# Performance work log

Measured on AMD Instinct MI355X. Metric: run time of the kernel, lower is better.

The kernel has to match this reference:

```python
import jax, jax.numpy as jnp
import numpy as np

TEMPERATURE = 0.1
EPS = 1e-12  # matches torch F.normalize default eps


def setup_inputs() -> dict:
    key = jax.random.key(0)
    k1, k2 = jax.random.split(key)
    B, D = 4096, 512
    features1 = jax.random.normal(k1, (B, D), dtype=jnp.float32)
    features2 = jax.random.normal(k2, (B, D), dtype=jnp.float32)
    return {"features1": features1, "features2": features2}


def _l2_normalize(x, axis=1):
    norm = jnp.linalg.norm(x, axis=axis, keepdims=True)
    return x / jnp.maximum(norm, EPS)


def reference(features1, features2):
    B = features1.shape[0]
    f1 = _l2_normalize(features1)
    f2 = _l2_normalize(features2)
    features = jnp.concatenate([f1, f2], axis=0)  # (2B, D)
    sim = jnp.matmul(features, features.T) / TEMPERATURE  # (2B, 2B)
    # mask self-similarity on the diagonal with -inf
    diag = jnp.eye(2 * B, dtype=bool)
    sim = jnp.where(diag, -jnp.inf, sim)
    # positive pair labels: row i pairs with i+B (first half) / i-B (second half)
    labels = jnp.concatenate([jnp.arange(B) + B, jnp.arange(B)], axis=0)
    log_probs = jax.nn.log_softmax(sim, axis=-1)  # (2B, 2B)
    nll = -jnp.take_along_axis(log_probs, labels[:, None], axis=1)[:, 0]
    return jnp.mean(nll)
```

## Files before the change

### kernel.cpp

```cpp
#include <hip/hip_runtime.h>

#define NROWS 8192
#define HALF_N 4096
#define DIM 512
#define INV_T 10.0f
#define NRB 64
#define NBLOCKS 2080

typedef __attribute__((ext_vector_type(4))) float f32x4;
typedef __attribute__((ext_vector_type(2))) long long2v;

__device__ __forceinline__ void async16(const void* g, void* l) {
  __builtin_amdgcn_global_load_lds(
      (const __attribute__((address_space(1))) unsigned int*)g,
      (__attribute__((address_space(3))) unsigned int*)l, 16, 0, 0);
}

__global__ __launch_bounds__(256) void norm_cast_k(
    const float* __restrict__ f1, const float* __restrict__ f2,
    unsigned char* __restrict__ Fa, unsigned char* __restrict__ Fb,
    float* __restrict__ rowsum, float* __restrict__ out) {
  int wave = threadIdx.x >> 6;
  int lane = threadIdx.x & 63;
  int row = blockIdx.x * 4 + wave;
  const float* src = (row < HALF_N) ? (f1 + (size_t)row * DIM)
                                    : (f2 + (size_t)(row - HALF_N) * DIM);
  const float4* p = reinterpret_cast<const float4*>(src + lane * 8);
  float4 v0 = p[0];
  float4 v1 = p[1];
  float ss = v0.x*v0.x + v0.y*v0.y + v0.z*v0.z + v0.w*v0.w
           + v1.x*v1.x + v1.y*v1.y + v1.z*v1.z + v1.w*v1.w;
  #pragma unroll
  for (int off = 1; off < 64; off <<= 1) ss += __shfl_xor(ss, off);
  float scale = 1.0f / fmaxf(sqrtf(ss), 1e-12f);
  int lo = __builtin_amdgcn_cvt_pk_fp8_f32(v0.x * scale, v0.y * scale, 0, false);
  lo = __builtin_amdgcn_cvt_pk_fp8_f32(v0.z * scale, v0.w * scale, lo, true);
  int hi = __builtin_amdgcn_cvt_pk_fp8_f32(v1.x * scale, v1.y * scale, 0, false);
  hi = __builtin_amdgcn_cvt_pk_fp8_f32(v1.z * scale, v1.w * scale, hi, true);
  int2 val = make_int2(lo, hi);
  int u = lane & 7;
  int g = lane >> 3;
  int pos = 2 * (u & 3) + (u >> 2);
  *reinterpret_cast<int2*>(Fb + (size_t)row * DIM + g * 64 + pos * 8) = val;
  int chunk = g * 4 + (u & 3);
  int slot = u >> 2;
  *reinterpret_cast<int2*>(Fa + (size_t)(row >> 4) * 8192 + chunk * 256 +
                           (row & 15) * 16 + slot * 8) = val;
  if (lane == 0) rowsum[row] = 0.0f;
  if (blockIdx.x == 0 && threadIdx.x == 0) out[0] = 0.0f;
}

__global__ __launch_bounds__(256, 3) void sym_gemm_k(
    const unsigned char* __restrict__ Fa, const unsigned char* __restrict__ Fb,
    float* __restrict__ rowsum, float* __restrict__ pairsim) {
  int bx = blockIdx.x;
  int gbx = (bx & 7) * (NBLOCKS / 8) + (bx >> 3);
  int rb = 0, rem = gbx;
  while (rem >= NRB - rb) { rem -= NRB - rb; ++rb; }
  const int cb = rb + rem;
  const int row0 = rb * 128, col0 = cb * 128;

  const int tid = threadIdx.x;
  const int wave = tid >> 6;
  const int lane = tid & 63;
  const int quad = lane >> 4;
  const int colid = lane & 15;
  const int wr0 = (wave >> 1) * 64;
  const int wc0 = (wave & 1) * 64;

  __shared__ __align__(16) unsigned char Blds[2][128 * 64];
  __shared__ float redrow[128];
  __shared__ float redcol[128];

  if (tid < 128) { redrow[tid] = 0.0f; redcol[tid] = 0.0f; }

  const unsigned char* srcB[2]; int dstO[2];
  #pragma unroll
  for (int seg = 0; seg < 2; ++seg) {
    int inst = wave + seg * 4;
    int r = inst * 16 + (lane >> 2);
    int c = (lane & 3) ^ ((r >> 1) & 3);
    srcB[seg] = Fb + (size_t)(col0 + r) * DIM + c * 16;
    dstO[seg] = inst * 1024;
  }

  const unsigned char* agp[4];
  #pragma unroll
  for (int t = 0; t < 4; ++t)
    agp[t] = Fa + (size_t)((row0 + wr0 + t * 16) >> 4) * 8192 +
             quad * 256 + colid * 16;

  int boff[4];
  #pragma unroll
  for (int t = 0; t < 4; ++t) {
    int rc = wc0 + t * 16 + colid;
    boff[t] = rc * 64 + ((quad ^ ((rc >> 1) & 3)) << 4);
  }

  f32x4 acc[4][4];
  #pragma unroll
  for (int t = 0; t < 4; ++t)
    #pragma unroll
    for (int u = 0; u < 4; ++u) acc[t][u] = (f32x4){0.f, 0.f, 0.f, 0.f};

  #pragma unroll
  for (int seg = 0; seg < 2; ++seg)
    async16(srcB[seg], &Blds[0][0] + dstO[seg]);
  long2v afc[4];
  #pragma unroll
  for (int t = 0; t < 4; ++t)
    afc[t] = *reinterpret_cast<const long2v*>(agp[t]);
  __syncthreads();

  #pragma unroll
  for (int kc = 0; kc < 8; ++kc) {
    const int cur = kc & 1;
    if (kc < 7) {
      #pragma unroll
      for (int seg = 0; seg < 2; ++seg)
        async16(srcB[seg] + (kc + 1) * 64, &Blds[cur ^ 1][0] + dstO[seg]);
    }
    long2v afn[4];
    if (kc < 7) {
      #pragma unroll
      for (int t = 0; t < 4; ++t)
        afn[t] = *reinterpret_cast<const long2v*>(agp[t] + (kc + 1) * 1024);
    }

    long2v bf[4];
    #pragma unroll
    for (int u = 0; u < 4; ++u)
      bf[u] = *reinterpret_cast<const long2v*>(&Blds[cur][0] + boff[u]);
    #pragma unroll
    for (int s = 0; s < 2; ++s)
      #pragma unroll
      for (int t = 0; t < 4; ++t)
        #pragma unroll
        for (int u = 0; u < 4; ++u)
          acc[t][u] = __builtin_amdgcn_mfma_f32_16x16x32_fp8_fp8(
              afc[t][s], bf[u][s], acc[t][u], 0, 0, 0);

    __syncthreads();
    if (kc < 7) {
      #pragma unroll
      for (int t = 0; t < 4; ++t) afc[t] = afn[t];
    }
  }

  float re[4][4];
  float ce[4];
  #pragma unroll
  for (int t = 0; t < 4; ++t)
    #pragma unroll
    for (int r = 0; r < 4; ++r) re[t][r] = 0.0f;
  #pragma unroll
  for (int u = 0; u < 4; ++u) ce[u] = 0.0f;

  #pragma unroll
  for (int t = 0; t < 4; ++t) {
    #pragma unroll
    for (int u = 0; u < 4; ++u) {
      f32x4 a = acc[t][u];
      const int gc = col0 + wc0 + u * 16 + colid;
      #pragma unroll
      for (int r = 0; r < 4; ++r) {
        int grow = row0 + wr0 + t * 16 + quad * 4 + r;
        float sim = a[r] * INV_T;
        float e = (gc > grow) ? __expf(sim) : 0.0f;
        re[t][r] += e;
        ce[u] += e;
        if (gc == grow + HALF_N && grow < HALF_N) {
          pairsim[grow] = sim;
          pairsim[gc] = sim;
        }
      }
    }
  }

  #pragma unroll
  for (int t = 0; t < 4; ++t)
    #pragma unroll
    for (int r = 0; r < 4; ++r) {
      float v = re[t][r];
      v += __shfl_xor(v, 1); v += __shfl_xor(v, 2);
      v += __shfl_xor(v, 4); v += __shfl_xor(v, 8);
      if (colid == 0) atomicAdd(&redrow[wr0 + t * 16 + quad * 4 + r], v);
    }
  #pragma unroll
  for (int u = 0; u < 4; ++u) {
    float v = ce[u];
    v += __shfl_xor(v, 16); v += __shfl_xor(v, 32);
    if (lane < 16) atomicAdd(&redcol[wc0 + u * 16 + colid], v);
  }
  __syncthreads();
  if (tid < 128) atomicAdd(&rowsum[row0 + tid], redrow[tid]);
  else           atomicAdd(&rowsum[col0 + tid - 128], redcol[tid - 128]);
}

__global__ __launch_bounds__(256) void finalize_k(
    const float* __restrict__ rowsum, const float* __restrict__ pairsim,
    float* __restrict__ out) {
  int i = blockIdx.x * 256 + threadIdx.x;
  float local = logf(rowsum[i]) - pairsim[i];
  #pragma unroll
  for (int off = 1; off < 64; off <<= 1) local += __shfl_xor(local, off);
  if ((threadIdx.x & 63) == 0)
    atomicAdd(out, local * (1.0f / (float)NROWS));
}

extern "C" void kernel_launch(void* const* d_in, const int* in_sizes, int n_in,
                              void* d_out, int out_size, void* d_ws, size_t ws_size,
                              hipStream_t stream) {
  const float* f1 = (const float*)d_in[0];
  const float* f2 = (const float*)d_in[1];
  unsigned char* Fa = (unsigned char*)d_ws;
  unsigned char* Fb = Fa + (size_t)NROWS * DIM;
  float* rowsum = (float*)(Fb + (size_t)NROWS * DIM);
  float* pairsim = rowsum + NROWS;
  float* out = (float*)d_out;

  norm_cast_k<<<NROWS / 4, 256, 0, stream>>>(f1, f2, Fa, Fb, rowsum, out);
  sym_gemm_k<<<NBLOCKS, 256, 0, stream>>>(Fa, Fb, rowsum, pairsim);
  finalize_k<<<NROWS / 256, 256, 0, stream>>>(rowsum, pairsim, out);
}
```

Baseline: 108.6 us.

## Enlarge symmetric GEMM tiles to 256x128 with 8 waves and 128-wide K chunks

Result: slower. 115.9 us (+6.7%).

```diff
diff --git a/kernel.cpp b/kernel.cpp
--- a/kernel.cpp
+++ b/kernel.cpp
@@ -4,8 +4,7 @@
 #define HALF_N 4096
 #define DIM 512
 #define INV_T 10.0f
-#define NRB 64
-#define NBLOCKS 2080
+#define NBLOCKS 1056
 
 typedef __attribute__((ext_vector_type(4))) float f32x4;
 typedef __attribute__((ext_vector_type(2))) long long2v;
@@ -50,15 +49,15 @@
   if (blockIdx.x == 0 && threadIdx.x == 0) out[0] = 0.0f;
 }
 
-__global__ __launch_bounds__(256, 3) void sym_gemm_k(
+__global__ __launch_bounds__(512, 4) void sym_gemm_k(
     const unsigned char* __restrict__ Fa, const unsigned char* __restrict__ Fb,
     float* __restrict__ rowsum, float* __restrict__ pairsim) {
   int bx = blockIdx.x;
   int gbx = (bx & 7) * (NBLOCKS / 8) + (bx >> 3);
   int rb = 0, rem = gbx;
-  while (rem >= NRB - rb) { rem -= NRB - rb; ++rb; }
-  const int cb = rb + rem;
-  const int row0 = rb * 128, col0 = cb * 128;
+  while (rem >= 64 - 2 * rb) { rem -= 64 - 2 * rb; ++rb; }
+  const int cb = 2 * rb + rem;
+  const int row0 = rb * 256, col0 = cb * 128;
 
   const int tid = threadIdx.x;
   const int wave = tid >> 6;
@@ -68,20 +67,23 @@
   const int wr0 = (wave >> 1) * 64;
   const int wc0 = (wave & 1) * 64;
 
-  __shared__ __align__(16) unsigned char Blds[2][128 * 64];
-  __shared__ float redrow[128];
+  __shared__ __align__(16) unsigned char Blds[2][128 * 128];
+  __shared__ float redrow[256];
   __shared__ float redcol[128];
 
-  if (tid < 128) { redrow[tid] = 0.0f; redcol[tid] = 0.0f; }
+  if (tid < 256) redrow[tid] = 0.0f;
+  if (tid < 128) redcol[tid] = 0.0f;
 
   const unsigned char* srcB[2]; int dstO[2];
-  #pragma unroll
-  for (int seg = 0; seg < 2; ++seg) {
-    int inst = wave + seg * 4;
-    int r = inst * 16 + (lane >> 2);
-    int c = (lane & 3) ^ ((r >> 1) & 3);
-    srcB[seg] = Fb + (size_t)(col0 + r) * DIM + c * 16;
-    dstO[seg] = inst * 1024;
+  {
+    int rloc = lane >> 3;
+    int l = (lane & 7) ^ rloc;
+    #pragma unroll
+    for (int seg = 0; seg < 2; ++seg) {
+      int inst = wave + seg * 8;
+      srcB[seg] = Fb + (size_t)(col0 + inst * 8 + rloc) * DIM + l * 16;
+      dstO[seg] = inst * 1024;
+    }
   }
 
   const unsigned char* agp[4];
@@ -90,11 +92,11 @@
     agp[t] = Fa + (size_t)((row0 + wr0 + t * 16) >> 4) * 8192 +
              quad * 256 + colid * 16;
 
-  int boff[4];
-  #pragma unroll
-  for (int t = 0; t < 4; ++t) {
-    int rc = wc0 + t * 16 + colid;
-    boff[t] = rc * 64 + ((quad ^ ((rc >> 1) & 3)) << 4);
+  int bq[4];
+  #pragma unroll
+  for (int u = 0; u < 4; ++u) {
+    int rc = wc0 + u * 16 + colid;
+    bq[u] = rc * 128 + ((quad ^ (colid & 7)) << 4);
   }
 
   f32x4 acc[4][4];
@@ -106,44 +108,35 @@
   #pragma unroll
   for (int seg = 0; seg < 2; ++seg)
     async16(srcB[seg], &Blds[0][0] + dstO[seg]);
-  long2v afc[4];
-  #pragma unroll
-  for (int t = 0; t < 4; ++t)
-    afc[t] = *reinterpret_cast<const long2v*>(agp[t]);
-  __syncthreads();
-
-  #pragma unroll
-  for (int kc = 0; kc < 8; ++kc) {
-    const int cur = kc & 1;
-    if (kc < 7) {
+
+  #pragma unroll
+  for (int kc = 0; kc < 4; ++kc) {
+    __syncthreads();
+    if (kc < 3) {
       #pragma unroll
       for (int seg = 0; seg < 2; ++seg)
-        async16(srcB[seg] + (kc + 1) * 64, &Blds[cur ^ 1][0] + dstO[seg]);
-    }
-    long2v afn[4];
-    if (kc < 7) {
+        async16(srcB[seg] + (kc + 1) * 128, &Blds[(kc & 1) ^ 1][0] + dstO[seg]);
+    }
+    #pragma unroll
+    for (int h = 0; h < 2; ++h) {
+      const int ss = kc * 2 + h;
+      long2v af[4];
       #pragma unroll
       for (int t = 0; t < 4; ++t)
-        afn[t] = *reinterpret_cast<const long2v*>(agp[t] + (kc + 1) * 1024);
-    }
-
-    long2v bf[4];
-    #pragma unroll
-    for (int u = 0; u < 4; ++u)
-      bf[u] = *reinterpret_cast<const long2v*>(&Blds[cur][0] + boff[u]);
-    #pragma unroll
-    for (int s = 0; s < 2; ++s)
-      #pragma unroll
-      for (int t = 0; t < 4; ++t)
+        af[t] = *reinterpret_cast<const long2v*>(agp[t] + ss * 1024);
+      long2v bf[4];
+      #pragma unroll
+      for (int u = 0; u < 4; ++u)
+        bf[u] = *reinterpret_cast<const long2v*>(
+            &Blds[kc & 1][0] + (bq[u] ^ (h << 6)));
+      #pragma unroll
+      for (int s = 0; s < 2; ++s)
         #pragma unroll
-        for (int u = 0; u < 4; ++u)
-          acc[t][u] = __builtin_amdgcn_mfma_f32_16x16x32_fp8_fp8(
-              afc[t][s], bf[u][s], acc[t][u], 0, 0, 0);
-
-    __syncthreads();
-    if (kc < 7) {
-      #pragma unroll
-      for (int t = 0; t < 4; ++t) afc[t] = afn[t];
+        for (int t = 0; t < 4; ++t)
+          #pragma unroll
+          for (int u = 0; u < 4; ++u)
+            acc[t][u] = __builtin_amdgcn_mfma_f32_16x16x32_fp8_fp8(
+                af[t][s], bf[u][s], acc[t][u], 0, 0, 0);
     }
   }
 
@@ -193,8 +186,8 @@
     if (lane < 16) atomicAdd(&redcol[wc0 + u * 16 + colid], v);
   }
   __syncthreads();
-  if (tid < 128) atomicAdd(&rowsum[row0 + tid], redrow[tid]);
-  else           atomicAdd(&rowsum[col0 + tid - 128], redcol[tid - 128]);
+  if (tid < 256)      atomicAdd(&rowsum[row0 + tid], redrow[tid]);
+  else if (tid < 384) atomicAdd(&rowsum[col0 + tid - 256], redcol[tid - 256]);
 }
 
 __global__ __launch_bounds__(256) void finalize_k(
@@ -220,6 +213,6 @@
   float* out = (float*)d_out;
 
   norm_cast_k<<<NROWS / 4, 256, 0, stream>>>(f1, f2, Fa, Fb, rowsum, out);
-  sym_gemm_k<<<NBLOCKS, 256, 0, stream>>>(Fa, Fb, rowsum, pairsim);
+  sym_gemm_k<<<NBLOCKS, 512, 0, stream>>>(Fa, Fb, rowsum, pairsim);
   finalize_k<<<NROWS / 256, 256, 0, stream>>>(rowsum, pairsim, out);
 }
```
